# Kernel optimization log

Hardware: AMD Instinct MI355X
Metric: run time of the kernel (lower is better)

Reference implementation:

```python
import jax, jax.numpy as jnp
import numpy as np

B, C, H, W = 512, 24, 56, 56  # x shape; hw = 3136 queries
M, D, DK = 49, 768, 24        # kv tokens, z dim, head dim
SCALE = DK ** (-0.5)


def setup_inputs() -> dict:
    key = jax.random.key(0)
    k1, k2, k3, k4, k5, k6 = jax.random.split(key, 6)
    x = jax.random.normal(k1, (B, C, H, W), dtype=jnp.float32)
    z = jax.random.normal(k2, (B, M, D), dtype=jnp.float32)
    # Linear(768, 24) params, stored as (in, out) for z @ W + b
    lim = 1.0 / np.sqrt(D)
    Wk = jax.random.uniform(k3, (D, DK), minval=-lim, maxval=lim, dtype=jnp.float32)
    bk = jax.random.uniform(k4, (DK,), minval=-lim, maxval=lim, dtype=jnp.float32)
    Wv = jax.random.uniform(k5, (D, DK), minval=-lim, maxval=lim, dtype=jnp.float32)
    bv = jax.random.uniform(k6, (DK,), minval=-lim, maxval=lim, dtype=jnp.float32)
    return {"x": x, "z": z, "Wk": Wk, "bk": bk, "Wv": Wv, "bv": bv}


def reference(x, z, Wk, bk, Wv, bv):
    b = x.shape[0]
    # q: (b, hw, c) -- flatten spatial, channels become the head dim
    q = x.reshape(b, C, H * W).transpose(0, 2, 1)
    k = z @ Wk + bk                      # (b, 49, 24)
    v = z @ Wv + bv                      # (b, 49, 24)
    dots = jnp.einsum('bqd,bmd->bqm', q, k) * SCALE  # (b, 3136, 49)
    attn = jax.nn.softmax(dots, axis=-1)
    out = jnp.einsum('bqm,bmd->bqd', attn, v)        # (b, 3136, 24)
    out = out.reshape(b, C, H, W)        # matches torch .view(b,24,56,56)
    return x + out
```

## Files before the change

kernel.cpp:

```cpp
#include <hip/hip_runtime.h>
#include <math.h>

#define B_   512
#define C_   24
#define HW_  3136
#define M_   49
#define D_   768
#define DK_  24
#define ROWS (B_*M_)
#define VOFF (ROWS*DK_)

#define KCHUNKS 4
#define KCH     (D_/KCHUNKS)
#define QBLK    13

__global__ __launch_bounds__(256) void init_kernel(
    const float* __restrict__ bk, const float* __restrict__ bv, float* __restrict__ kv)
{
    int i = blockIdx.x * 256 + threadIdx.x;
    if (i >= 2 * VOFF) return;
    int c = i % DK_;
    kv[i] = (i < VOFF) ? bk[c] : bv[c];
}

__global__ __launch_bounds__(128, 6) void proj_kernel(
    const float* __restrict__ z, const float* __restrict__ Wk,
    const float* __restrict__ Wv, float* __restrict__ kv)
{
    __shared__ float zt[64][36];
    __shared__ float wt[48][36];

    const int t     = threadIdx.x;
    const int tile  = blockIdx.x >> 2;
    const int chunk = blockIdx.x & 3;
    const int r0    = tile * 64;
    const int rb    = t & 15;
    const int c0    = (t >> 4) * 6;

    float acc[4][6];
    #pragma unroll
    for (int i = 0; i < 4; ++i)
        #pragma unroll
        for (int j = 0; j < 6; ++j) acc[i][j] = 0.f;

    for (int s = 0; s < KCH; s += 32) {
        const int kc = chunk * KCH + s;
        #pragma unroll
        for (int p = 0; p < 4; ++p) {
            int lin = p * 128 + t;
            int row = lin >> 3;
            int col = (lin & 7) * 4;
            const float4 zv = *(const float4*)(z + (size_t)(r0 + row) * D_ + kc + col);
            *(float4*)&zt[row][col] = zv;
        }
        #pragma unroll
        for (int i = 0; i < 12; ++i) {
            int idx = i * 128 + t;
            int d = idx & 31;
            int c = idx >> 5;
            wt[c][d] = (c < 24) ? Wk[(kc + d) * DK_ + c] : Wv[(kc + d) * DK_ + (c - 24)];
        }
        __syncthreads();
        #pragma unroll
        for (int k4 = 0; k4 < 8; ++k4) {
            float4 za[4], wa[6];
            #pragma unroll
            for (int i = 0; i < 4; ++i) za[i] = *(const float4*)&zt[rb + 16 * i][k4 * 4];
            #pragma unroll
            for (int j = 0; j < 6; ++j) wa[j] = *(const float4*)&wt[c0 + j][k4 * 4];
            #pragma unroll
            for (int i = 0; i < 4; ++i)
                #pragma unroll
                for (int j = 0; j < 6; ++j) {
                    acc[i][j] += za[i].x * wa[j].x;
                    acc[i][j] += za[i].y * wa[j].y;
                    acc[i][j] += za[i].z * wa[j].z;
                    acc[i][j] += za[i].w * wa[j].w;
                }
        }
        __syncthreads();
    }

    #pragma unroll
    for (int j = 0; j < 6; ++j) {
        int c = c0 + j;
        float* base = (c < 24) ? kv : (kv + VOFF);
        int cc = (c < 24) ? c : (c - 24);
        #pragma unroll
        for (int i = 0; i < 4; ++i) {
            int rg = r0 + rb + 16 * i;
            atomicAdd(&base[(size_t)rg * DK_ + cc], acc[i][j]);
        }
    }
}

__global__ __launch_bounds__(256, 6) void attn_kernel(
    const float* __restrict__ x, const float* __restrict__ kv, float* __restrict__ out)
{
    const int b  = blockIdx.x / QBLK;
    const int hw = (blockIdx.x % QBLK) * 256 + threadIdx.x;
    if (hw >= HW_) return;

    const float scale = 0.20412414523193154f;

    const float* xb = x + (size_t)b * (C_ * HW_);
    float q[C_];
    #pragma unroll
    for (int c = 0; c < C_; ++c) q[c] = xb[c * HW_ + hw] * scale;

    const float* kb = kv + (size_t)b * (M_ * DK_);
    const float* vb = kv + VOFF + (size_t)b * (M_ * DK_);

    float o[C_];
    #pragma unroll
    for (int c = 0; c < C_; ++c) o[c] = 0.f;
    float s = 0.f;

    #pragma unroll 1
    for (int m = 0; m < M_; ++m) {
        float a = 0.f;
        #pragma unroll
        for (int c = 0; c < DK_; ++c) a += q[c] * kb[m * DK_ + c];
        float p = __expf(a);
        s += p;
        #pragma unroll
        for (int c = 0; c < C_; ++c) o[c] += p * vb[m * DK_ + c];
    }
    const float inv = 1.f / s;

    const float* xr = xb + (size_t)hw * C_;
    float*       ob = out + (size_t)b * (C_ * HW_) + (size_t)hw * C_;
    #pragma unroll
    for (int c4 = 0; c4 < C_; c4 += 4) {
        float4 xv = *(const float4*)(xr + c4);
        float4 ov;
        ov.x = xv.x + o[c4+0] * inv;
        ov.y = xv.y + o[c4+1] * inv;
        ov.z = xv.z + o[c4+2] * inv;
        ov.w = xv.w + o[c4+3] * inv;
        *(float4*)(ob + c4) = ov;
    }
}

extern "C" void kernel_launch(void* const* d_in, const int* in_sizes, int n_in,
                              void* d_out, int out_size, void* d_ws, size_t ws_size,
                              hipStream_t stream) {
    const float* x  = (const float*)d_in[0];
    const float* z  = (const float*)d_in[1];
    const float* Wk = (const float*)d_in[2];
    const float* bk = (const float*)d_in[3];
    const float* Wv = (const float*)d_in[4];
    const float* bv = (const float*)d_in[5];
    float* out = (float*)d_out;
    float* kv  = (float*)d_ws;

    init_kernel<<<(2 * VOFF + 255) / 256, 256, 0, stream>>>(bk, bv, kv);
    proj_kernel<<<(ROWS / 64) * KCHUNKS, 128, 0, stream>>>(z, Wk, Wv, kv);
    attn_kernel<<<B_ * QBLK, 256, 0, stream>>>(x, kv, out);
}
```

Baseline: 515.8 us.

## Replace atomic split-K projection with partial buffers and a reduction kernel

The projection kernel now writes per-chunk partial sums with plain vector stores into a scratch buffer, which reuses the output array, instead of doing atomicAdd into the kv buffer. A new reduce kernel sums the 8 partials and adds the biases, so the init kernel is no longer needed. The split-K factor goes from 4 to 8 to give more blocks. This removes atomic contention, but it adds extra global traffic for the partials and one more launch. It depends on the output buffer being large enough to hold the scratch partials before the attention kernel overwrites it.

Result: faster. 450.5 us (-12.7%).

```diff
diff --git a/kernel.cpp b/kernel.cpp
--- a/kernel.cpp
+++ b/kernel.cpp
@@ -10,29 +10,22 @@
 #define ROWS (B_*M_)
 #define VOFF (ROWS*DK_)
 
-#define KCHUNKS 4
+#define KCHUNKS 8
 #define KCH     (D_/KCHUNKS)
 #define QBLK    13
-
-__global__ __launch_bounds__(256) void init_kernel(
-    const float* __restrict__ bk, const float* __restrict__ bv, float* __restrict__ kv)
-{
-    int i = blockIdx.x * 256 + threadIdx.x;
-    if (i >= 2 * VOFF) return;
-    int c = i % DK_;
-    kv[i] = (i < VOFF) ? bk[c] : bv[c];
-}
+#define PCOLS   48
+#define PSTRIDE ((size_t)ROWS * PCOLS)
 
 __global__ __launch_bounds__(128, 6) void proj_kernel(
     const float* __restrict__ z, const float* __restrict__ Wk,
-    const float* __restrict__ Wv, float* __restrict__ kv)
+    const float* __restrict__ Wv, float* __restrict__ part)
 {
     __shared__ float zt[64][36];
     __shared__ float wt[48][36];
 
     const int t     = threadIdx.x;
-    const int tile  = blockIdx.x >> 2;
-    const int chunk = blockIdx.x & 3;
+    const int tile  = blockIdx.x >> 3;
+    const int chunk = blockIdx.x & 7;
     const int r0    = tile * 64;
     const int rb    = t & 15;
     const int c0    = (t >> 4) * 6;
@@ -82,16 +75,31 @@
     }
 
     #pragma unroll
-    for (int j = 0; j < 6; ++j) {
-        int c = c0 + j;
-        float* base = (c < 24) ? kv : (kv + VOFF);
-        int cc = (c < 24) ? c : (c - 24);
+    for (int i = 0; i < 4; ++i) {
+        float* base = part + (size_t)chunk * PSTRIDE
+                           + (size_t)(r0 + rb + 16 * i) * PCOLS + c0;
         #pragma unroll
-        for (int i = 0; i < 4; ++i) {
-            int rg = r0 + rb + 16 * i;
-            atomicAdd(&base[(size_t)rg * DK_ + cc], acc[i][j]);
+        for (int j = 0; j < 6; j += 2) {
+            float2 v2 = make_float2(acc[i][j], acc[i][j + 1]);
+            *(float2*)(base + j) = v2;
         }
     }
+}
+
+__global__ __launch_bounds__(256) void reduce_kernel(
+    const float* __restrict__ part, const float* __restrict__ bk,
+    const float* __restrict__ bv, float* __restrict__ kv)
+{
+    int i = blockIdx.x * 256 + threadIdx.x;
+    int row = i / PCOLS;
+    int c   = i - row * PCOLS;
+
+    float v = 0.f;
+    #pragma unroll
+    for (int k = 0; k < KCHUNKS; ++k) v += part[(size_t)k * PSTRIDE + i];
+
+    if (c < DK_) kv[(size_t)row * DK_ + c]               = v + bk[c];
+    else         kv[VOFF + (size_t)row * DK_ + (c - DK_)] = v + bv[c - DK_];
 }
 
 __global__ __launch_bounds__(256, 6) void attn_kernel(
@@ -151,10 +159,11 @@
     const float* bk = (const float*)d_in[3];
     const float* Wv = (const float*)d_in[4];
     const float* bv = (const float*)d_in[5];
-    float* out = (float*)d_out;
-    float* kv  = (float*)d_ws;
+    float* out  = (float*)d_out;
+    float* part = (float*)d_out;
+    float* kv   = (float*)d_ws;
 
-    init_kernel<<<(2 * VOFF + 255) / 256, 256, 0, stream>>>(bk, bv, kv);
-    proj_kernel<<<(ROWS / 64) * KCHUNKS, 128, 0, stream>>>(z, Wk, Wv, kv);
+    proj_kernel<<<(ROWS / 64) * KCHUNKS, 128, 0, stream>>>(z, Wk, Wv, part);
+    reduce_kernel<<<(ROWS * PCOLS) / 256, 256, 0, stream>>>(part, bk, bv, kv);
     attn_kernel<<<B_ * QBLK, 256, 0, stream>>>(x, kv, out);
 }
```
